# Optimization experiments

Measured on AMD Instinct MI355X. Metric: run time of the kernel, lower is better.

The kernel has to match this reference:

```python
import jax, jax.numpy as jnp
import numpy as np

N = 20000
IN_CH = 256
HID = 32
HEADS = 8
OUT_CH = 40
NEG_SLOPE = 0.2


def _gat_layer(x, src, dst, W, a_src, a_dst, b, heads, ch, concat):
    # x: [N, F_in], W: [F_in, heads*ch], a_src/a_dst: [heads, ch], b: [heads*ch] or [ch]
    n = x.shape[0]
    h = (x @ W).reshape(n, heads, ch)                      # [N, H, C]
    alpha_s = jnp.einsum('nhc,hc->nh', h, a_src)           # [N, H]
    alpha_d = jnp.einsum('nhc,hc->nh', h, a_dst)           # [N, H]
    e = jax.nn.leaky_relu(alpha_s[src] + alpha_d[dst], NEG_SLOPE)  # [E, H]
    # segment softmax over edges sharing the same destination node
    m = jax.ops.segment_max(e, dst, num_segments=n)        # [N, H]
    ex = jnp.exp(e - m[dst])                               # [E, H]
    denom = jax.ops.segment_sum(ex, dst, num_segments=n)   # [N, H]
    alpha = ex / (denom[dst] + 1e-16)                      # [E, H]
    out = jax.ops.segment_sum(h[src] * alpha[:, :, None], dst, num_segments=n)  # [N, H, C]
    out = out.reshape(n, heads * ch) if concat else out.mean(axis=1)
    return out + b


def setup_inputs() -> dict:
    key = jax.random.key(0)
    ks = jax.random.split(key, 12)
    x = jax.random.normal(ks[0], (N, IN_CH), dtype=jnp.float32)
    edge_index = jax.random.randint(ks[1], (2, 320000), 0, N, dtype=jnp.int64)
    s1 = 1.0 / np.sqrt(IN_CH)
    s2 = 1.0 / np.sqrt(HEADS * HID)
    W1 = jax.random.uniform(ks[2], (IN_CH, HEADS * HID), jnp.float32, -s1, s1)
    a1_src = jax.random.uniform(ks[3], (HEADS, HID), jnp.float32, -s2, s2)
    a1_dst = jax.random.uniform(ks[4], (HEADS, HID), jnp.float32, -s2, s2)
    b1 = jnp.zeros((HEADS * HID,), jnp.float32)
    W2 = jax.random.uniform(ks[5], (HEADS * HID, OUT_CH), jnp.float32, -s2, s2)
    so = 1.0 / np.sqrt(OUT_CH)
    a2_src = jax.random.uniform(ks[6], (1, OUT_CH), jnp.float32, -so, so)
    a2_dst = jax.random.uniform(ks[7], (1, OUT_CH), jnp.float32, -so, so)
    b2 = jnp.zeros((OUT_CH,), jnp.float32)
    return {"x": x, "edge_index": edge_index, "W1": W1, "a1_src": a1_src,
            "a1_dst": a1_dst, "b1": b1, "W2": W2, "a2_src": a2_src,
            "a2_dst": a2_dst, "b2": b2}


def reference(x, edge_index, W1, a1_src, a1_dst, b1, W2, a2_src, a2_dst, b2):
    n = x.shape[0]
    loop = jnp.arange(n, dtype=edge_index.dtype)
    src = jnp.concatenate([edge_index[0], loop])  # PyG adds self-loops by default
    dst = jnp.concatenate([edge_index[1], loop])
    # dropout layers are identity in eval mode
    h = _gat_layer(x, src, dst, W1, a1_src, a1_dst, b1, HEADS, HID, concat=True)
    h = jax.nn.elu(h)
    out = _gat_layer(h, src, dst, W2, a2_src, a2_dst, b2, 1, OUT_CH, concat=False)
    return jax.nn.log_softmax(out, axis=1)
```

## Files before the change

kernel.cpp:

```cpp
#include <hip/hip_runtime.h>
#include <math.h>

#define N_NODES 20000
#define N_PAD   20032
#define E_RAW   320000
#define E_TOT   (E_RAW + N_NODES)
#define IN_CH   256
#define HEADS   8
#define HID     32
#define HH      (HEADS*HID)
#define OUT_CH  40
#define NC2     48
#define NEG     0.2f
#define CSTRIDE 64

#define HIST_BLKS ((E_TOT + 255) / 256)
#define XB_BLKS   (N_NODES / 8)
#define G1_BLKS   313

typedef __attribute__((ext_vector_type(8))) short  short8;
typedef __attribute__((ext_vector_type(4))) float  floatx4;

__device__ __forceinline__ unsigned short f2bf(float f) {
    unsigned int u = __float_as_uint(f);
    unsigned int r = (u + 0x7FFFu + ((u >> 16) & 1u)) >> 16;
    return (unsigned short)r;
}
__device__ __forceinline__ float bf2f(unsigned short h) {
    return __uint_as_float(((unsigned int)h) << 16);
}
__device__ __forceinline__ float lexp(float v) {
    v = (v > 0.f) ? v : NEG * v;
    return __expf(v);
}

__device__ __forceinline__ void gload16(const void* g, void* l) {
    __builtin_amdgcn_global_load_lds(
        (const __attribute__((address_space(1))) void*)g,
        (__attribute__((address_space(3))) void*)l, 16, 0, 0);
}


__global__ void setup_hist(const int* __restrict__ ei,
                           const float* __restrict__ x,
                           const float* __restrict__ W1,
                           const float* __restrict__ W2,
                           unsigned short* __restrict__ w1t,
                           unsigned short* __restrict__ w2t,
                           unsigned short* __restrict__ xb,
                           int* __restrict__ deg,
                           int* __restrict__ pos) {
    int b = blockIdx.x;
    int t = threadIdx.x;
    if (b < HIST_BLKS) {
        int e = b * 256 + t;
        if (e >= E_TOT) return;
        int d = (e < E_RAW) ? ei[E_RAW + e] : (e - E_RAW);
        pos[e] = atomicAdd(&deg[d], 1);
    } else if (b < HIST_BLKS + HH) {
        int c = b - HIST_BLKS;
        w1t[c * IN_CH + t] = f2bf(W1[(size_t)t * HH + c]);
    } else if (b < HIST_BLKS + HH + NC2) {
        int c = b - HIST_BLKS - HH;
        w2t[c * HH + t] = (c < OUT_CH) ? f2bf(W2[(size_t)t * OUT_CH + c]) : (unsigned short)0;
    } else {
        int bb = b - (HIST_BLKS + HH + NC2);
        int n = bb * 8 + (t >> 5);
        int c0 = (t & 31) * 8;
        const float4* src = reinterpret_cast<const float4*>(&x[(size_t)n * IN_CH + c0]);
        float4 v0 = src[0], v1 = src[1];
        short8 sv;
        sv[0] = (short)f2bf(v0.x); sv[1] = (short)f2bf(v0.y);
        sv[2] = (short)f2bf(v0.z); sv[3] = (short)f2bf(v0.w);
        sv[4] = (short)f2bf(v1.x); sv[5] = (short)f2bf(v1.y);
        sv[6] = (short)f2bf(v1.z); sv[7] = (short)f2bf(v1.w);
        *reinterpret_cast<short8*>(&xb[(size_t)n * IN_CH + c0]) = sv;
    }
}

__global__ __launch_bounds__(256) void gemm1(const unsigned short* __restrict__ xb,
                                             const unsigned short* __restrict__ w1t,
                                             const float* __restrict__ a1s,
                                             const float* __restrict__ a1d,
                                             unsigned short* __restrict__ h1b,
                                             float* __restrict__ as1,
                                             float* __restrict__ ad1,
                                             const int* __restrict__ ei,
                                             const int* __restrict__ pos,
                                             int* __restrict__ csr) {
    __shared__ unsigned char Al[64 * 512];
    __shared__ unsigned char Bl[256 * 128];
    int t = threadIdx.x;

    if (blockIdx.x >= G1_BLKS) {
        int e = (blockIdx.x - G1_BLKS) * 256 + t;
        if (e < E_TOT) {
            int s, d;
            if (e < E_RAW) { s = ei[e]; d = ei[E_RAW + e]; }
            else           { s = e - E_RAW; d = s; }
            int pp = pos[e];
            if (pp < CSTRIDE) csr[d * CSTRIDE + pp] = s;
        }
        return;
    }

    int wave = t >> 6, lane = t & 63;
    int ln = lane & 15, q = lane >> 4;
    int n0 = blockIdx.x * 64;
    const char* xbase = (const char*)xb + (size_t)n0 * 512;
    const char* bbase = (const char*)w1t;

    #pragma unroll
    for (int j = 0; j < 8; j++) {
        int R = (wave * 8 + j) * 1024;
        int o = R + lane * 16;
        int r = o >> 9;
        int cb = (o & 511) ^ ((r & 7) << 4);
        gload16(xbase + (size_t)r * 512 + cb, &Al[R]);
    }
    #pragma unroll
    for (int j = 0; j < 8; j++) {
        int R = (wave * 8 + j) * 1024;
        int o = R + lane * 16;
        int r = o >> 7;
        int cb = (o & 127) ^ ((r & 7) << 4);
        gload16(bbase + (size_t)r * 512 + cb, &Bl[R]);
    }
    __syncthreads();

    floatx4 acc[16];
    #pragma unroll
    for (int f = 0; f < 16; f++) acc[f] = (floatx4){0.f, 0.f, 0.f, 0.f};

    int xorv = (ln & 7) << 4;

    for (int c = 0; c < 4; c++) {
        #pragma unroll
        for (int ks = 0; ks < 2; ks++) {
            int ao = (16 * wave + ln) * 512 + c * 128 + ((ks * 64 + q * 16) ^ xorv);
            short8 a = *reinterpret_cast<const short8*>(&Al[ao]);
            int bo0 = ln * 128 + ((ks * 64 + q * 16) ^ xorv);
            #pragma unroll
            for (int f = 0; f < 16; f++) {
                short8 bfr = *reinterpret_cast<const short8*>(&Bl[bo0 + f * 2048]);
                acc[f] = __builtin_amdgcn_mfma_f32_16x16x32_bf16(a, bfr, acc[f], 0, 0, 0);
            }
        }
        if (c < 3) {
            __syncthreads();
            #pragma unroll
            for (int j = 0; j < 8; j++) {
                int R = (wave * 8 + j) * 1024;
                int o = R + lane * 16;
                int r = o >> 7;
                int cb = (o & 127) ^ ((r & 7) << 4);
                gload16(bbase + (size_t)r * 512 + (c + 1) * 128 + cb, &Bl[R]);
            }
            __syncthreads();
        }
    }

    float Asr[16], Adr[16];
    #pragma unroll
    for (int f = 0; f < 16; f++) {
        Asr[f] = a1s[16 * f + ln];
        Adr[f] = a1d[16 * f + ln];
    }
    #pragma unroll
    for (int f = 0; f < 16; f++) {
        #pragma unroll
        for (int r = 0; r < 4; r++) {
            int n = n0 + 16 * wave + q * 4 + r;
            if (n < N_NODES)
                h1b[(size_t)n * HH + 16 * f + ln] = f2bf(acc[f][r]);
        }
    }
    #pragma unroll
    for (int lh = 0; lh < 8; lh++) {
        #pragma unroll
        for (int r = 0; r < 4; r++) {
            float ps = acc[2*lh][r] * Asr[2*lh] + acc[2*lh+1][r] * Asr[2*lh+1];
            float pd = acc[2*lh][r] * Adr[2*lh] + acc[2*lh+1][r] * Adr[2*lh+1];
            ps += __shfl_xor(ps, 1); ps += __shfl_xor(ps, 2);
            ps += __shfl_xor(ps, 4); ps += __shfl_xor(ps, 8);
            pd += __shfl_xor(pd, 1); pd += __shfl_xor(pd, 2);
            pd += __shfl_xor(pd, 4); pd += __shfl_xor(pd, 8);
            int n = n0 + 16 * wave + q * 4 + r;
            if (ln == 0 && n < N_NODES) {
                as1[n * HEADS + lh] = ps;
                ad1[n * HEADS + lh] = pd;
            }
        }
    }
}


__global__ __launch_bounds__(256) void aggr1(const unsigned short* __restrict__ h1b,
                                             const float* __restrict__ as1,
                                             const float* __restrict__ ad1,
                                             const float* __restrict__ b1,
                                             const int* __restrict__ degv,
                                             const int* __restrict__ csr,
                                             unsigned short* __restrict__ h2b) {
    int d = blockIdx.x * 4 + (threadIdx.x >> 6);
    int lane = threadIdx.x & 63;
    int h = lane >> 3;
    int c4 = lane * 4;
    int start = d * CSTRIDE;
    int deg = degv[d];
    deg = (deg > CSTRIDE) ? CSTRIDE : deg;
    float adv = ad1[d * HEADS + h];

    float a0 = 0.f, a1 = 0.f, a2 = 0.f, a3 = 0.f, den = 0.f;
    int jj = 0;
    for (; jj + 8 <= deg; jj += 8) {
        int s[8];
        #pragma unroll
        for (int i = 0; i < 8; i++) s[i] = csr[start + jj + i];
        float e[8];
        #pragma unroll
        for (int i = 0; i < 8; i++) e[i] = as1[s[i] * HEADS + h];
        ushort4 pv[8];
        #pragma unroll
        for (int i = 0; i < 8; i++)
            pv[i] = *reinterpret_cast<const ushort4*>(&h1b[(size_t)s[i] * HH + c4]);
        #pragma unroll
        for (int i = 0; i < 8; i++) {
            float w = lexp(e[i] + adv);
            den += w;
            a0 = fmaf(bf2f(pv[i].x), w, a0);
            a1 = fmaf(bf2f(pv[i].y), w, a1);
            a2 = fmaf(bf2f(pv[i].z), w, a2);
            a3 = fmaf(bf2f(pv[i].w), w, a3);
        }
    }
    for (; jj < deg; jj++) {
        int s = csr[start + jj];
        float w = lexp(as1[s * HEADS + h] + adv);
        den += w;
        ushort4 pv = *reinterpret_cast<const ushort4*>(&h1b[(size_t)s * HH + c4]);
        a0 = fmaf(bf2f(pv.x), w, a0);
        a1 = fmaf(bf2f(pv.y), w, a1);
        a2 = fmaf(bf2f(pv.z), w, a2);
        a3 = fmaf(bf2f(pv.w), w, a3);
    }
    float inv = 1.0f / (den + 1e-16f);
    float4 bv = *reinterpret_cast<const float4*>(&b1[c4]);
    float r0 = a0 * inv + bv.x;
    float r1 = a1 * inv + bv.y;
    float r2 = a2 * inv + bv.z;
    float r3 = a3 * inv + bv.w;
    r0 = (r0 > 0.f) ? r0 : (__expf(r0) - 1.f);
    r1 = (r1 > 0.f) ? r1 : (__expf(r1) - 1.f);
    r2 = (r2 > 0.f) ? r2 : (__expf(r2) - 1.f);
    r3 = (r3 > 0.f) ? r3 : (__expf(r3) - 1.f);
    ushort4 ov;
    ov.x = f2bf(r0); ov.y = f2bf(r1); ov.z = f2bf(r2); ov.w = f2bf(r3);
    *reinterpret_cast<ushort4*>(&h2b[(size_t)d * HH + c4]) = ov;
}


__global__ __launch_bounds__(256) void gemm2(const unsigned short* __restrict__ h2b,
                                             const unsigned short* __restrict__ w2t,
                                             const float* __restrict__ a2s,
                                             const float* __restrict__ a2d,
                                             unsigned short* __restrict__ h3b,
                                             float* __restrict__ as2,
                                             float* __restrict__ ad2) {
    __shared__ unsigned char Al[64 * 512];
    __shared__ unsigned char Bl[NC2 * 512];
    int t = threadIdx.x;
    int wave = t >> 6, lane = t & 63;
    int ln = lane & 15, q = lane >> 4;
    int n0 = blockIdx.x * 64;
    const char* abase = (const char*)h2b + (size_t)n0 * 512;
    const char* bbase = (const char*)w2t;

    #pragma unroll
    for (int j = 0; j < 8; j++) {
        int R = (wave * 8 + j) * 1024;
        int o = R + lane * 16;
        int r = o >> 9;
        int cb = (o & 511) ^ ((r & 7) << 4);
        gload16(abase + (size_t)r * 512 + cb, &Al[R]);
    }
    #pragma unroll
    for (int j = 0; j < 6; j++) {
        int R = (wave * 6 + j) * 1024;
        int o = R + lane * 16;
        int r = o >> 9;
        int cb = (o & 511) ^ ((r & 7) << 4);
        gload16(bbase + (size_t)r * 512 + cb, &Bl[R]);
    }
    __syncthreads();

    floatx4 acc[3];
    #pragma unroll
    for (int f = 0; f < 3; f++) acc[f] = (floatx4){0.f, 0.f, 0.f, 0.f};

    int xorv = (ln & 7) << 4;

    #pragma unroll
    for (int kf = 0; kf < 8; kf++) {
        int ao = ((16 * wave + ln) * 512 + kf * 64 + q * 16) ^ xorv;
        short8 a = *reinterpret_cast<const short8*>(&Al[ao]);
        int bo0 = (ln * 512 + kf * 64 + q * 16) ^ xorv;
        #pragma unroll
        for (int f = 0; f < 3; f++) {
            short8 bfr = *reinterpret_cast<const short8*>(&Bl[bo0 + f * 8192]);
            acc[f] = __builtin_amdgcn_mfma_f32_16x16x32_bf16(a, bfr, acc[f], 0, 0, 0);
        }
    }

    float a2sv[3], a2dv[3];
    #pragma unroll
    for (int f = 0; f < 3; f++) {
        int c = 16 * f + ln;
        a2sv[f] = (c < OUT_CH) ? a2s[c] : 0.f;
        a2dv[f] = (c < OUT_CH) ? a2d[c] : 0.f;
    }
    #pragma unroll
    for (int r = 0; r < 4; r++) {
        int n = n0 + 16 * wave + q * 4 + r;
        float ps = acc[0][r] * a2sv[0] + acc[1][r] * a2sv[1] + acc[2][r] * a2sv[2];
        float pd = acc[0][r] * a2dv[0] + acc[1][r] * a2dv[1] + acc[2][r] * a2dv[2];
        ps += __shfl_xor(ps, 1); ps += __shfl_xor(ps, 2);
        ps += __shfl_xor(ps, 4); ps += __shfl_xor(ps, 8);
        pd += __shfl_xor(pd, 1); pd += __shfl_xor(pd, 2);
        pd += __shfl_xor(pd, 4); pd += __shfl_xor(pd, 8);
        if (n < N_NODES) {
            #pragma unroll
            for (int f = 0; f < 3; f++) {
                int c = 16 * f + ln;
                if (c < OUT_CH)
                    h3b[(size_t)n * OUT_CH + c] = f2bf(acc[f][r]);
            }
            if (ln == 0) { as2[n] = ps; ad2[n] = pd; }
        }
    }
}


__global__ __launch_bounds__(256) void aggr2(const unsigned short* __restrict__ h3b,
                                             const float* __restrict__ as2,
                                             const float* __restrict__ ad2,
                                             const float* __restrict__ b2,
                                             const int* __restrict__ degv,
                                             const int* __restrict__ csr,
                                             float* __restrict__ out) {
    int d = blockIdx.x * 4 + (threadIdx.x >> 6);
    int lane = threadIdx.x & 63;
    int start = d * CSTRIDE;
    int deg = degv[d];
    deg = (deg > CSTRIDE) ? CSTRIDE : deg;
    float adv = ad2[d];
    bool ok = (lane < OUT_CH);
    int cl = ok ? lane : 0;

    float acc = 0.f, den = 0.f;
    int jj = 0;
    for (; jj + 8 <= deg; jj += 8) {
        int s[8];
        #pragma unroll
        for (int i = 0; i < 8; i++) s[i] = csr[start + jj + i];
        float e[8];
        #pragma unroll
        for (int i = 0; i < 8; i++) e[i] = as2[s[i]];
        unsigned short qv[8];
        #pragma unroll
        for (int i = 0; i < 8; i++) qv[i] = h3b[(size_t)s[i] * OUT_CH + cl];
        #pragma unroll
        for (int i = 0; i < 8; i++) {
            float w = lexp(e[i] + adv);
            den += w;
            acc = fmaf(bf2f(qv[i]), w, acc);
        }
    }
    for (; jj < deg; jj++) {
        int s = csr[start + jj];
        float w = lexp(as2[s] + adv);
        den += w;
        acc = fmaf(bf2f(h3b[(size_t)s * OUT_CH + cl]), w, acc);
    }

    float r = ok ? (acc / (den + 1e-16f) + b2[lane]) : -1e30f;
    float mx = r;
    #pragma unroll
    for (int off = 32; off >= 1; off >>= 1) mx = fmaxf(mx, __shfl_xor(mx, off));
    float ex = ok ? __expf(r - mx) : 0.f;
    float se = ex;
    #pragma unroll
    for (int off = 32; off >= 1; off >>= 1) se += __shfl_xor(se, off);
    if (ok) out[(size_t)d * OUT_CH + lane] = r - mx - __logf(se);
}


extern "C" void kernel_launch(void* const* d_in, const int* in_sizes, int n_in,
                              void* d_out, int out_size, void* d_ws, size_t ws_size,
                              hipStream_t stream) {
    const float* x   = (const float*)d_in[0];
    const int*   ei  = (const int*)  d_in[1];
    const float* W1  = (const float*)d_in[2];
    const float* a1s = (const float*)d_in[3];
    const float* a1d = (const float*)d_in[4];
    const float* b1  = (const float*)d_in[5];
    const float* W2  = (const float*)d_in[6];
    const float* a2s = (const float*)d_in[7];
    const float* a2d = (const float*)d_in[8];
    const float* b2  = (const float*)d_in[9];
    float* out = (float*)d_out;

    char* p = (char*)d_ws;
    auto alloc = [&](size_t bytes) {
        char* r = p;
        p += (bytes + 255) & ~(size_t)255;
        return r;
    };
    unsigned short* xb  = (unsigned short*)alloc((size_t)N_PAD * IN_CH * 2);
    unsigned short* h1b = (unsigned short*)alloc((size_t)N_NODES * HH * 2);
    unsigned short* h2b = (unsigned short*)alloc((size_t)N_PAD * HH * 2);
    unsigned short* h3b = (unsigned short*)alloc((size_t)N_NODES * OUT_CH * 2);
    unsigned short* w1t = (unsigned short*)alloc((size_t)IN_CH * HH * 2);
    unsigned short* w2t = (unsigned short*)alloc((size_t)NC2 * HH * 2);
    float* as1  = (float*)alloc((size_t)N_NODES * HEADS * 4);
    float* ad1  = (float*)alloc((size_t)N_NODES * HEADS * 4);
    float* as2v = (float*)alloc((size_t)N_NODES * 4);
    float* ad2v = (float*)alloc((size_t)N_NODES * 4);
    int* deg    = (int*)alloc((size_t)N_NODES * 4);
    int* pos    = (int*)alloc((size_t)E_TOT * 4);
    int* csr    = (int*)alloc((size_t)N_NODES * CSTRIDE * 4);

    hipMemsetAsync(deg, 0, (size_t)N_NODES * sizeof(int), stream);
    setup_hist<<<HIST_BLKS + HH + NC2 + XB_BLKS, 256, 0, stream>>>(
        ei, x, W1, W2, w1t, w2t, xb, deg, pos);
    gemm1<<<G1_BLKS + HIST_BLKS, 256, 0, stream>>>(xb, w1t, a1s, a1d, h1b, as1, ad1,
                                                   ei, pos, csr);
    aggr1<<<N_NODES / 4, 256, 0, stream>>>(h1b, as1, ad1, b1, deg, csr, h2b);
    gemm2<<<313, 256, 0, stream>>>(h2b, w2t, a2s, a2d, h3b, as2v, ad2v);
    aggr2<<<N_NODES / 4, 256, 0, stream>>>(h3b, as2v, ad2v, b2, deg, csr, out);
}
```

Before: 169.4 us.

## Fuse layer-1 aggregation into layer-2 GEMM and build CSR with atomics

Merges the first-layer attention aggregation and the second-layer GEMM into one 512-thread kernel that writes aggregated rows straight into swizzled LDS and then runs MFMA on them, removing the h2b round trip and one launch. The separate histogram pass and pos array are dropped: gemm1's tail blocks now take CSR slots directly with atomicAdd on deg, and deg is zeroed inside the prep kernel instead of a memset. The trade-off is far fewer blocks for aggregation (313 blocks of 8 waves versus 5000 blocks), so gather-latency hiding may suffer, and only half the waves take part in the MFMA stage.

Result: slower. 179.7 us (+6.1%).

```diff
diff --git a/kernel.cpp b/kernel.cpp
--- a/kernel.cpp
+++ b/kernel.cpp
@@ -14,6 +14,7 @@
 #define NEG     0.2f
 #define CSTRIDE 64
 
+#define ZB_BLKS   79
 #define HIST_BLKS ((E_TOT + 255) / 256)
 #define XB_BLKS   (N_NODES / 8)
 #define G1_BLKS   313
@@ -41,30 +42,26 @@
 }
 
 
-__global__ void setup_hist(const int* __restrict__ ei,
-                           const float* __restrict__ x,
+__global__ void setup_prep(const float* __restrict__ x,
                            const float* __restrict__ W1,
                            const float* __restrict__ W2,
                            unsigned short* __restrict__ w1t,
                            unsigned short* __restrict__ w2t,
                            unsigned short* __restrict__ xb,
-                           int* __restrict__ deg,
-                           int* __restrict__ pos) {
+                           int* __restrict__ deg) {
     int b = blockIdx.x;
     int t = threadIdx.x;
-    if (b < HIST_BLKS) {
-        int e = b * 256 + t;
-        if (e >= E_TOT) return;
-        int d = (e < E_RAW) ? ei[E_RAW + e] : (e - E_RAW);
-        pos[e] = atomicAdd(&deg[d], 1);
-    } else if (b < HIST_BLKS + HH) {
-        int c = b - HIST_BLKS;
+    if (b < ZB_BLKS) {
+        int i = b * 256 + t;
+        if (i < N_NODES) deg[i] = 0;
+    } else if (b < ZB_BLKS + HH) {
+        int c = b - ZB_BLKS;
         w1t[c * IN_CH + t] = f2bf(W1[(size_t)t * HH + c]);
-    } else if (b < HIST_BLKS + HH + NC2) {
-        int c = b - HIST_BLKS - HH;
+    } else if (b < ZB_BLKS + HH + NC2) {
+        int c = b - ZB_BLKS - HH;
         w2t[c * HH + t] = (c < OUT_CH) ? f2bf(W2[(size_t)t * OUT_CH + c]) : (unsigned short)0;
     } else {
-        int bb = b - (HIST_BLKS + HH + NC2);
+        int bb = b - (ZB_BLKS + HH + NC2);
         int n = bb * 8 + (t >> 5);
         int c0 = (t & 31) * 8;
         const float4* src = reinterpret_cast<const float4*>(&x[(size_t)n * IN_CH + c0]);
@@ -86,7 +83,7 @@
                                              float* __restrict__ as1,
                                              float* __restrict__ ad1,
                                              const int* __restrict__ ei,
-                                             const int* __restrict__ pos,
+                                             int* __restrict__ deg,
                                              int* __restrict__ csr) {
     __shared__ unsigned char Al[64 * 512];
     __shared__ unsigned char Bl[256 * 128];
@@ -98,8 +95,8 @@
             int s, d;
             if (e < E_RAW) { s = ei[e]; d = ei[E_RAW + e]; }
             else           { s = e - E_RAW; d = s; }
-            int pp = pos[e];
-            if (pp < CSTRIDE) csr[d * CSTRIDE + pp] = s;
+            int slot = atomicAdd(&deg[d], 1);
+            if (slot < CSTRIDE) csr[d * CSTRIDE + slot] = s;
         }
         return;
     }
@@ -195,147 +192,141 @@
 }
 
 
-__global__ __launch_bounds__(256) void aggr1(const unsigned short* __restrict__ h1b,
-                                             const float* __restrict__ as1,
-                                             const float* __restrict__ ad1,
-                                             const float* __restrict__ b1,
-                                             const int* __restrict__ degv,
-                                             const int* __restrict__ csr,
-                                             unsigned short* __restrict__ h2b) {
-    int d = blockIdx.x * 4 + (threadIdx.x >> 6);
-    int lane = threadIdx.x & 63;
-    int h = lane >> 3;
-    int c4 = lane * 4;
-    int start = d * CSTRIDE;
-    int deg = degv[d];
-    deg = (deg > CSTRIDE) ? CSTRIDE : deg;
-    float adv = ad1[d * HEADS + h];
-
-    float a0 = 0.f, a1 = 0.f, a2 = 0.f, a3 = 0.f, den = 0.f;
-    int jj = 0;
-    for (; jj + 8 <= deg; jj += 8) {
-        int s[8];
-        #pragma unroll
-        for (int i = 0; i < 8; i++) s[i] = csr[start + jj + i];
-        float e[8];
-        #pragma unroll
-        for (int i = 0; i < 8; i++) e[i] = as1[s[i] * HEADS + h];
-        ushort4 pv[8];
-        #pragma unroll
-        for (int i = 0; i < 8; i++)
-            pv[i] = *reinterpret_cast<const ushort4*>(&h1b[(size_t)s[i] * HH + c4]);
-        #pragma unroll
-        for (int i = 0; i < 8; i++) {
-            float w = lexp(e[i] + adv);
-            den += w;
-            a0 = fmaf(bf2f(pv[i].x), w, a0);
-            a1 = fmaf(bf2f(pv[i].y), w, a1);
-            a2 = fmaf(bf2f(pv[i].z), w, a2);
-            a3 = fmaf(bf2f(pv[i].w), w, a3);
-        }
-    }
-    for (; jj < deg; jj++) {
-        int s = csr[start + jj];
-        float w = lexp(as1[s * HEADS + h] + adv);
-        den += w;
-        ushort4 pv = *reinterpret_cast<const ushort4*>(&h1b[(size_t)s * HH + c4]);
-        a0 = fmaf(bf2f(pv.x), w, a0);
-        a1 = fmaf(bf2f(pv.y), w, a1);
-        a2 = fmaf(bf2f(pv.z), w, a2);
-        a3 = fmaf(bf2f(pv.w), w, a3);
-    }
-    float inv = 1.0f / (den + 1e-16f);
-    float4 bv = *reinterpret_cast<const float4*>(&b1[c4]);
-    float r0 = a0 * inv + bv.x;
-    float r1 = a1 * inv + bv.y;
-    float r2 = a2 * inv + bv.z;
-    float r3 = a3 * inv + bv.w;
-    r0 = (r0 > 0.f) ? r0 : (__expf(r0) - 1.f);
-    r1 = (r1 > 0.f) ? r1 : (__expf(r1) - 1.f);
-    r2 = (r2 > 0.f) ? r2 : (__expf(r2) - 1.f);
-    r3 = (r3 > 0.f) ? r3 : (__expf(r3) - 1.f);
-    ushort4 ov;
-    ov.x = f2bf(r0); ov.y = f2bf(r1); ov.z = f2bf(r2); ov.w = f2bf(r3);
-    *reinterpret_cast<ushort4*>(&h2b[(size_t)d * HH + c4]) = ov;
-}
-
-
-__global__ __launch_bounds__(256) void gemm2(const unsigned short* __restrict__ h2b,
-                                             const unsigned short* __restrict__ w2t,
-                                             const float* __restrict__ a2s,
-                                             const float* __restrict__ a2d,
-                                             unsigned short* __restrict__ h3b,
-                                             float* __restrict__ as2,
-                                             float* __restrict__ ad2) {
+__global__ __launch_bounds__(512) void l2fused(const unsigned short* __restrict__ h1b,
+                                               const float* __restrict__ as1,
+                                               const float* __restrict__ ad1,
+                                               const float* __restrict__ b1,
+                                               const int* __restrict__ degv,
+                                               const int* __restrict__ csr,
+                                               const unsigned short* __restrict__ w2t,
+                                               const float* __restrict__ a2s,
+                                               const float* __restrict__ a2d,
+                                               unsigned short* __restrict__ h3b,
+                                               float* __restrict__ as2,
+                                               float* __restrict__ ad2) {
     __shared__ unsigned char Al[64 * 512];
     __shared__ unsigned char Bl[NC2 * 512];
     int t = threadIdx.x;
-    int wave = t >> 6, lane = t & 63;
-    int ln = lane & 15, q = lane >> 4;
+    int wv = t >> 6, lane = t & 63;
     int n0 = blockIdx.x * 64;
-    const char* abase = (const char*)h2b + (size_t)n0 * 512;
-    const char* bbase = (const char*)w2t;
-
-    #pragma unroll
-    for (int j = 0; j < 8; j++) {
-        int R = (wave * 8 + j) * 1024;
+
+    #pragma unroll
+    for (int j = 0; j < 3; j++) {
+        int R = (wv * 3 + j) * 1024;
         int o = R + lane * 16;
         int r = o >> 9;
         int cb = (o & 511) ^ ((r & 7) << 4);
-        gload16(abase + (size_t)r * 512 + cb, &Al[R]);
-    }
-    #pragma unroll
-    for (int j = 0; j < 6; j++) {
-        int R = (wave * 6 + j) * 1024;
-        int o = R + lane * 16;
-        int r = o >> 9;
-        int cb = (o & 511) ^ ((r & 7) << 4);
-        gload16(bbase + (size_t)r * 512 + cb, &Bl[R]);
+        gload16((const char*)w2t + (size_t)r * 512 + cb, &Bl[R]);
+    }
+
+    int h = lane >> 3;
+    int c4 = lane * 4;
+    for (int i = 0; i < 8; i++) {
+        int rr = wv * 8 + i;
+        int d = n0 + rr;
+        ushort4 ov;
+        if (d < N_NODES) {
+            int start = d * CSTRIDE;
+            int deg = degv[d];
+            deg = (deg > CSTRIDE) ? CSTRIDE : deg;
+            float adv = ad1[d * HEADS + h];
+            float a0 = 0.f, a1 = 0.f, a2 = 0.f, a3 = 0.f, den = 0.f;
+            int jj = 0;
+            for (; jj + 8 <= deg; jj += 8) {
+                int s[8];
+                #pragma unroll
+                for (int k = 0; k < 8; k++) s[k] = csr[start + jj + k];
+                float e[8];
+                #pragma unroll
+                for (int k = 0; k < 8; k++) e[k] = as1[s[k] * HEADS + h];
+                ushort4 pv[8];
+                #pragma unroll
+                for (int k = 0; k < 8; k++)
+                    pv[k] = *reinterpret_cast<const ushort4*>(&h1b[(size_t)s[k] * HH + c4]);
+                #pragma unroll
+                for (int k = 0; k < 8; k++) {
+                    float w = lexp(e[k] + adv);
+                    den += w;
+                    a0 = fmaf(bf2f(pv[k].x), w, a0);
+                    a1 = fmaf(bf2f(pv[k].y), w, a1);
+                    a2 = fmaf(bf2f(pv[k].z), w, a2);
+                    a3 = fmaf(bf2f(pv[k].w), w, a3);
+                }
+            }
+            for (; jj < deg; jj++) {
+                int s = csr[start + jj];
+                float w = lexp(as1[s * HEADS + h] + adv);
+                den += w;
+                ushort4 pv = *reinterpret_cast<const ushort4*>(&h1b[(size_t)s * HH + c4]);
+                a0 = fmaf(bf2f(pv.x), w, a0);
+                a1 = fmaf(bf2f(pv.y), w, a1);
+                a2 = fmaf(bf2f(pv.z), w, a2);
+                a3 = fmaf(bf2f(pv.w), w, a3);
+            }
+            float inv = 1.0f / (den + 1e-16f);
+            float4 bv = *reinterpret_cast<const float4*>(&b1[c4]);
+            float r0 = a0 * inv + bv.x;
+            float r1 = a1 * inv + bv.y;
+            float r2 = a2 * inv + bv.z;
+            float r3 = a3 * inv + bv.w;
+            r0 = (r0 > 0.f) ? r0 : (__expf(r0) - 1.f);
+            r1 = (r1 > 0.f) ? r1 : (__expf(r1) - 1.f);
+            r2 = (r2 > 0.f) ? r2 : (__expf(r2) - 1.f);
+            r3 = (r3 > 0.f) ? r3 : (__expf(r3) - 1.f);
+            ov.x = f2bf(r0); ov.y = f2bf(r1); ov.z = f2bf(r2); ov.w = f2bf(r3);
+        } else {
+            ov.x = 0; ov.y = 0; ov.z = 0; ov.w = 0;
+        }
+        int base = (rr * 512 + lane * 8) ^ ((rr & 7) << 4);
+        *reinterpret_cast<ushort4*>(&Al[base]) = ov;
     }
     __syncthreads();
 
-    floatx4 acc[3];
-    #pragma unroll
-    for (int f = 0; f < 3; f++) acc[f] = (floatx4){0.f, 0.f, 0.f, 0.f};
-
-    int xorv = (ln & 7) << 4;
-
-    #pragma unroll
-    for (int kf = 0; kf < 8; kf++) {
-        int ao = ((16 * wave + ln) * 512 + kf * 64 + q * 16) ^ xorv;
-        short8 a = *reinterpret_cast<const short8*>(&Al[ao]);
-        int bo0 = (ln * 512 + kf * 64 + q * 16) ^ xorv;
-        #pragma unroll
-        for (int f = 0; f < 3; f++) {
-            short8 bfr = *reinterpret_cast<const short8*>(&Bl[bo0 + f * 8192]);
-            acc[f] = __builtin_amdgcn_mfma_f32_16x16x32_bf16(a, bfr, acc[f], 0, 0, 0);
-        }
-    }
-
-    float a2sv[3], a2dv[3];
-    #pragma unroll
-    for (int f = 0; f < 3; f++) {
-        int c = 16 * f + ln;
-        a2sv[f] = (c < OUT_CH) ? a2s[c] : 0.f;
-        a2dv[f] = (c < OUT_CH) ? a2d[c] : 0.f;
-    }
-    #pragma unroll
-    for (int r = 0; r < 4; r++) {
-        int n = n0 + 16 * wave + q * 4 + r;
-        float ps = acc[0][r] * a2sv[0] + acc[1][r] * a2sv[1] + acc[2][r] * a2sv[2];
-        float pd = acc[0][r] * a2dv[0] + acc[1][r] * a2dv[1] + acc[2][r] * a2dv[2];
-        ps += __shfl_xor(ps, 1); ps += __shfl_xor(ps, 2);
-        ps += __shfl_xor(ps, 4); ps += __shfl_xor(ps, 8);
-        pd += __shfl_xor(pd, 1); pd += __shfl_xor(pd, 2);
-        pd += __shfl_xor(pd, 4); pd += __shfl_xor(pd, 8);
-        if (n < N_NODES) {
+    if (wv < 4) {
+        int ln = lane & 15, q = lane >> 4;
+        floatx4 acc[3];
+        #pragma unroll
+        for (int f = 0; f < 3; f++) acc[f] = (floatx4){0.f, 0.f, 0.f, 0.f};
+
+        int xorv = (ln & 7) << 4;
+
+        #pragma unroll
+        for (int kf = 0; kf < 8; kf++) {
+            int ao = ((16 * wv + ln) * 512 + kf * 64 + q * 16) ^ xorv;
+            short8 a = *reinterpret_cast<const short8*>(&Al[ao]);
+            int bo0 = (ln * 512 + kf * 64 + q * 16) ^ xorv;
             #pragma unroll
             for (int f = 0; f < 3; f++) {
-                int c = 16 * f + ln;
-                if (c < OUT_CH)
-                    h3b[(size_t)n * OUT_CH + c] = f2bf(acc[f][r]);
-            }
-            if (ln == 0) { as2[n] = ps; ad2[n] = pd; }
+                short8 bfr = *reinterpret_cast<const short8*>(&Bl[bo0 + f * 8192]);
+                acc[f] = __builtin_amdgcn_mfma_f32_16x16x32_bf16(a, bfr, acc[f], 0, 0, 0);
+            }
+        }
+
+        float a2sv[3], a2dv[3];
+        #pragma unroll
+        for (int f = 0; f < 3; f++) {
+            int c = 16 * f + ln;
+            a2sv[f] = (c < OUT_CH) ? a2s[c] : 0.f;
+            a2dv[f] = (c < OUT_CH) ? a2d[c] : 0.f;
+        }
+        #pragma unroll
+        for (int r = 0; r < 4; r++) {
+            int n = n0 + 16 * wv + q * 4 + r;
+            float ps = acc[0][r] * a2sv[0] + acc[1][r] * a2sv[1] + acc[2][r] * a2sv[2];
+            float pd = acc[0][r] * a2dv[0] + acc[1][r] * a2dv[1] + acc[2][r] * a2dv[2];
+            ps += __shfl_xor(ps, 1); ps += __shfl_xor(ps, 2);
+            ps += __shfl_xor(ps, 4); ps += __shfl_xor(ps, 8);
+            pd += __shfl_xor(pd, 1); pd += __shfl_xor(pd, 2);
+            pd += __shfl_xor(pd, 4); pd += __shfl_xor(pd, 8);
+            if (n < N_NODES) {
+                #pragma unroll
+                for (int f = 0; f < 3; f++) {
+                    int c = 16 * f + ln;
+                    if (c < OUT_CH)
+                        h3b[(size_t)n * OUT_CH + c] = f2bf(acc[f][r]);
+                }
+                if (ln == 0) { as2[n] = ps; ad2[n] = pd; }
+            }
         }
     }
 }
@@ -418,7 +409,6 @@
     };
     unsigned short* xb  = (unsigned short*)alloc((size_t)N_PAD * IN_CH * 2);
     unsigned short* h1b = (unsigned short*)alloc((size_t)N_NODES * HH * 2);
-    unsigned short* h2b = (unsigned short*)alloc((size_t)N_PAD * HH * 2);
     unsigned short* h3b = (unsigned short*)alloc((size_t)N_NODES * OUT_CH * 2);
     unsigned short* w1t = (unsigned short*)alloc((size_t)IN_CH * HH * 2);
     unsigned short* w2t = (unsigned short*)alloc((size_t)NC2 * HH * 2);
@@ -427,15 +417,13 @@
     float* as2v = (float*)alloc((size_t)N_NODES * 4);
     float* ad2v = (float*)alloc((size_t)N_NODES * 4);
     int* deg    = (int*)alloc((size_t)N_NODES * 4);
-    int* pos    = (int*)alloc((size_t)E_TOT * 4);
     int* csr    = (int*)alloc((size_t)N_NODES * CSTRIDE * 4);
 
-    hipMemsetAsync(deg, 0, (size_t)N_NODES * sizeof(int), stream);
-    setup_hist<<<HIST_BLKS + HH + NC2 + XB_BLKS, 256, 0, stream>>>(
-        ei, x, W1, W2, w1t, w2t, xb, deg, pos);
+    setup_prep<<<ZB_BLKS + HH + NC2 + XB_BLKS, 256, 0, stream>>>(
+        x, W1, W2, w1t, w2t, xb, deg);
     gemm1<<<G1_BLKS + HIST_BLKS, 256, 0, stream>>>(xb, w1t, a1s, a1d, h1b, as1, ad1,
-                                                   ei, pos, csr);
-    aggr1<<<N_NODES / 4, 256, 0, stream>>>(h1b, as1, ad1, b1, deg, csr, h2b);
-    gemm2<<<313, 256, 0, stream>>>(h2b, w2t, a2s, a2d, h3b, as2v, ad2v);
+                                                   ei, deg, csr);
+    l2fused<<<G1_BLKS, 512, 0, stream>>>(h1b, as1, ad1, b1, deg, csr,
+                                         w2t, a2s, a2d, h3b, as2v, ad2v);
     aggr2<<<N_NODES / 4, 256, 0, stream>>>(h3b, as2v, ad2v, b2, deg, csr, out);
 }
```

## Fold degree histogram into CSR fill and zero degrees in setup kernel

Applied to the files above, without the earlier changes.

Removes the separate histogram pass that stored per-edge positions: the CSR scatter blocks in gemm1 now take slots directly with an atomicAdd on the degree counter. The degree array is zeroed inside the setup kernel instead of by a separate memset. This drops one edge pass, the pos array traffic and a memset launch. In exchange the slot order within each destination becomes nondeterministic, so floating-point summation order in the aggregation can vary between runs.

Result: faster. 161.3 us (-4.8%).

```diff
diff --git a/kernel.cpp b/kernel.cpp
--- a/kernel.cpp
+++ b/kernel.cpp
@@ -14,6 +14,7 @@
 #define NEG     0.2f
 #define CSTRIDE 64
 
+#define ZB_BLKS   79
 #define HIST_BLKS ((E_TOT + 255) / 256)
 #define XB_BLKS   (N_NODES / 8)
 #define G1_BLKS   313
@@ -41,30 +42,26 @@
 }
 
 
-__global__ void setup_hist(const int* __restrict__ ei,
-                           const float* __restrict__ x,
+__global__ void setup_prep(const float* __restrict__ x,
                            const float* __restrict__ W1,
                            const float* __restrict__ W2,
                            unsigned short* __restrict__ w1t,
                            unsigned short* __restrict__ w2t,
                            unsigned short* __restrict__ xb,
-                           int* __restrict__ deg,
-                           int* __restrict__ pos) {
+                           int* __restrict__ deg) {
     int b = blockIdx.x;
     int t = threadIdx.x;
-    if (b < HIST_BLKS) {
-        int e = b * 256 + t;
-        if (e >= E_TOT) return;
-        int d = (e < E_RAW) ? ei[E_RAW + e] : (e - E_RAW);
-        pos[e] = atomicAdd(&deg[d], 1);
-    } else if (b < HIST_BLKS + HH) {
-        int c = b - HIST_BLKS;
+    if (b < ZB_BLKS) {
+        int i = b * 256 + t;
+        if (i < N_NODES) deg[i] = 0;
+    } else if (b < ZB_BLKS + HH) {
+        int c = b - ZB_BLKS;
         w1t[c * IN_CH + t] = f2bf(W1[(size_t)t * HH + c]);
-    } else if (b < HIST_BLKS + HH + NC2) {
-        int c = b - HIST_BLKS - HH;
+    } else if (b < ZB_BLKS + HH + NC2) {
+        int c = b - ZB_BLKS - HH;
         w2t[c * HH + t] = (c < OUT_CH) ? f2bf(W2[(size_t)t * OUT_CH + c]) : (unsigned short)0;
     } else {
-        int bb = b - (HIST_BLKS + HH + NC2);
+        int bb = b - (ZB_BLKS + HH + NC2);
         int n = bb * 8 + (t >> 5);
         int c0 = (t & 31) * 8;
         const float4* src = reinterpret_cast<const float4*>(&x[(size_t)n * IN_CH + c0]);
@@ -86,7 +83,7 @@
                                              float* __restrict__ as1,
                                              float* __restrict__ ad1,
                                              const int* __restrict__ ei,
-                                             const int* __restrict__ pos,
+                                             int* __restrict__ deg,
                                              int* __restrict__ csr) {
     __shared__ unsigned char Al[64 * 512];
     __shared__ unsigned char Bl[256 * 128];
@@ -98,8 +95,8 @@
             int s, d;
             if (e < E_RAW) { s = ei[e]; d = ei[E_RAW + e]; }
             else           { s = e - E_RAW; d = s; }
-            int pp = pos[e];
-            if (pp < CSTRIDE) csr[d * CSTRIDE + pp] = s;
+            int slot = atomicAdd(&deg[d], 1);
+            if (slot < CSTRIDE) csr[d * CSTRIDE + slot] = s;
         }
         return;
     }
@@ -427,14 +424,12 @@
     float* as2v = (float*)alloc((size_t)N_NODES * 4);
     float* ad2v = (float*)alloc((size_t)N_NODES * 4);
     int* deg    = (int*)alloc((size_t)N_NODES * 4);
-    int* pos    = (int*)alloc((size_t)E_TOT * 4);
     int* csr    = (int*)alloc((size_t)N_NODES * CSTRIDE * 4);
 
-    hipMemsetAsync(deg, 0, (size_t)N_NODES * sizeof(int), stream);
-    setup_hist<<<HIST_BLKS + HH + NC2 + XB_BLKS, 256, 0, stream>>>(
-        ei, x, W1, W2, w1t, w2t, xb, deg, pos);
+    setup_prep<<<ZB_BLKS + HH + NC2 + XB_BLKS, 256, 0, stream>>>(
+        x, W1, W2, w1t, w2t, xb, deg);
     gemm1<<<G1_BLKS + HIST_BLKS, 256, 0, stream>>>(xb, w1t, a1s, a1d, h1b, as1, ad1,
-                                                   ei, pos, csr);
+                                                   ei, deg, csr);
     aggr1<<<N_NODES / 4, 256, 0, stream>>>(h1b, as1, ad1, b1, deg, csr, h2b);
     gemm2<<<313, 256, 0, stream>>>(h2b, w2t, a2s, a2d, h3b, as2v, ad2v);
     aggr2<<<N_NODES / 4, 256, 0, stream>>>(h3b, as2v, ad2v, b2, deg, csr, out);
```
